# Optimization experiments

Measured on AMD Instinct MI355X. Metric: run time of the kernel, lower is better.

The kernel has to match this reference:

```python
import jax, jax.numpy as jnp
import numpy as np

TAU_U = 1.0
TAU_L = 0.05
EPS = 1e-12  # torch F.normalize eps


def setup_inputs() -> dict:
    key = jax.random.key(0)
    ks = jax.random.split(key, 8)
    N, D, B = 100000, 128, 8192
    x1 = jax.random.normal(ks[0], (N, D), dtype=jnp.float32)
    x2 = jax.random.normal(ks[1], (N, D), dtype=jnp.float32)
    x1_index = jax.random.randint(ks[2], (B,), 0, N, dtype=jnp.int64 if jax.config.jax_enable_x64 else jnp.int32)
    x2_index = jax.random.randint(ks[3], (B,), 0, N, dtype=jnp.int64 if jax.config.jax_enable_x64 else jnp.int32)
    # Linear params (torch Linear default init: U(-1/sqrt(fan_in), 1/sqrt(fan_in)))
    lim1 = 1.0 / np.sqrt(D)
    W1 = jax.random.uniform(ks[4], (D, D), minval=-lim1, maxval=lim1, dtype=jnp.float32)
    b1 = jax.random.uniform(ks[5], (D,), minval=-lim1, maxval=lim1, dtype=jnp.float32)
    W2 = jax.random.uniform(ks[6], (1, D), minval=-lim1, maxval=lim1, dtype=jnp.float32)
    b2 = jax.random.uniform(ks[7], (1,), minval=-lim1, maxval=lim1, dtype=jnp.float32)
    return {"x1": x1, "x2": x2, "x1_index": x1_index, "x2_index": x2_index,
            "W1": W1, "b1": b1, "W2": W2, "b2": b2}


def _l2norm(x):
    # matches torch F.normalize(dim=1) for 2-D input
    n = jnp.sqrt(jnp.sum(x * x, axis=-1, keepdims=True))
    return x / jnp.maximum(n, EPS)


def reference(x1, x2, x1_index, x2_index, W1, b1, W2, b2):
    x1_feat = _l2norm(x1[x1_index])          # [B, D]
    x2_feat = _l2norm(x2[x2_index])          # [B, D]

    h = x1_feat * x2_feat                    # [B, D]
    h = h @ W1.T + b1                        # lin1
    h = jnp.where(h >= 0, h, 0.2 * h)        # leaky_relu(0.2)
    s = jax.nn.sigmoid(h @ W2.T + b2)        # [B, 1]
    ssl_temp = (TAU_U - TAU_L) * (1.0 - s) + TAU_L   # [B, 1]

    pos = jnp.sum(x1_feat * x2_feat, axis=-1)         # [B]
    # NOTE: [B] / [B,1] broadcasts to [B,B] exactly like torch
    pos_rating = jnp.exp(pos / ssl_temp)              # [B, B]

    tot = x1_feat @ x2_feat.T                          # [B, B]
    tot_rating = jnp.sum(jnp.exp(tot / ssl_temp), axis=1)  # [B]

    ssl_temp_avg = jnp.mean(ssl_temp)
    return (pos_rating, tot_rating, ssl_temp_avg)
```

## Files before the change

kernel.cpp:

```cpp
#include <hip/hip_runtime.h>
#include <stdint.h>

typedef __bf16 bf16x8 __attribute__((ext_vector_type(8)));
typedef float f32x4 __attribute__((ext_vector_type(4)));
typedef __attribute__((address_space(3))) uint32_t as3u32;
typedef const __attribute__((address_space(1))) uint32_t as1u32;

#define B_TOT 8192
#define DD 128
#define OUT_TOT 67108864UL
#define OUT_AVG 67117056UL

__device__ inline unsigned short f2bf(float x){
  union { float f; uint32_t u; } v; v.f = x;
  return (unsigned short)((v.u + 0x7fffu + ((v.u >> 16) & 1u)) >> 16);
}

__global__ __launch_bounds__(256) void k_feat(const float* __restrict__ x1,
    const float* __restrict__ x2, const int* __restrict__ i1a, const int* __restrict__ i2a,
    unsigned short* __restrict__ f1b, unsigned short* __restrict__ f2b,
    unsigned short* __restrict__ hb, float* __restrict__ posw, float* __restrict__ out){
  int tid = threadIdx.x;
  int gid = blockIdx.x * 256 + tid;
  if (gid <= 8192) out[OUT_TOT + gid] = 0.f;
  int w = tid >> 6, l = tid & 63;
  int b = blockIdx.x * 4 + w;
  const float2* r1 = (const float2*)(x1 + (size_t)i1a[b] * DD);
  const float2* r2 = (const float2*)(x2 + (size_t)i2a[b] * DD);
  float2 v1 = r1[l], v2 = r2[l];
  float s1 = v1.x * v1.x + v1.y * v1.y;
  float s2 = v2.x * v2.x + v2.y * v2.y;
  #pragma unroll
  for (int o = 32; o; o >>= 1){ s1 += __shfl_xor(s1, o); s2 += __shfl_xor(s2, o); }
  float inv1 = 1.f / fmaxf(sqrtf(s1), 1e-12f);
  float inv2 = 1.f / fmaxf(sqrtf(s2), 1e-12f);
  float f1x = v1.x * inv1, f1y = v1.y * inv1;
  float f2x = v2.x * inv2, f2y = v2.y * inv2;
  float hx = f1x * f2x, hy = f1y * f2y;
  float ps = hx + hy;
  #pragma unroll
  for (int o = 32; o; o >>= 1) ps += __shfl_xor(ps, o);
  unsigned int u1 = (unsigned int)f2bf(f1x) | ((unsigned int)f2bf(f1y) << 16);
  unsigned int u2 = (unsigned int)f2bf(f2x) | ((unsigned int)f2bf(f2y) << 16);
  unsigned int uh = (unsigned int)f2bf(hx)  | ((unsigned int)f2bf(hy)  << 16);
  ((unsigned int*)f1b)[b * 64 + l] = u1;
  ((unsigned int*)f2b)[b * 64 + l] = u2;
  ((unsigned int*)hb)[b * 64 + l]  = uh;
  if (l == 0) posw[b] = ps;
}

__device__ inline void stage_tile(const unsigned short* g, unsigned short* s){
  int tid = threadIdx.x;
  #pragma unroll
  for (int it = 0; it < 8; ++it){
    int c = tid + it * 256;
    int row = c >> 4, cc = c & 15;
    int src = (row << 4) + (cc ^ (row & 7));
    __builtin_amdgcn_global_load_lds((as1u32*)(g + src * 8),
                                     (as3u32*)(s + c * 8), 16, 0, 0);
  }
}

__device__ inline void mfma_tile(const unsigned short* As, const unsigned short* Bs,
                                 f32x4 acc[4][4]){
  int tid = threadIdx.x;
  int w = tid >> 6, l = tid & 63;
  int wr = (w >> 1) * 64, wc = (w & 1) * 64;
  int lo = l & 15, hi = l >> 4;
  f32x4 zero = {0.f, 0.f, 0.f, 0.f};
  #pragma unroll
  for (int m = 0; m < 4; ++m)
    #pragma unroll
    for (int n = 0; n < 4; ++n) acc[m][n] = zero;
  #pragma unroll
  for (int kk = 0; kk < 4; ++kk){
    bf16x8 af[4], bfv[4];
    #pragma unroll
    for (int m = 0; m < 4; ++m){
      int row = wr + m * 16 + lo;
      af[m] = *(const bf16x8*)(As + row * 128 + ((kk * 4 + hi) ^ (row & 7)) * 8);
    }
    #pragma unroll
    for (int n = 0; n < 4; ++n){
      int row = wc + n * 16 + lo;
      bfv[n] = *(const bf16x8*)(Bs + row * 128 + ((kk * 4 + hi) ^ (row & 7)) * 8);
    }
    #pragma unroll
    for (int m = 0; m < 4; ++m)
      #pragma unroll
      for (int n = 0; n < 4; ++n)
        acc[m][n] = __builtin_amdgcn_mfma_f32_16x16x32_bf16(af[m], bfv[n], acc[m][n], 0, 0, 0);
  }
}

__global__ __launch_bounds__(256) void k_lin(const unsigned short* __restrict__ hb,
    const float* __restrict__ W1, const float* __restrict__ b1,
    const float* __restrict__ W2, const float* __restrict__ b2,
    float* __restrict__ rTw, float* __restrict__ out){
  __shared__ __align__(16) unsigned short As[16384];
  __shared__ __align__(16) unsigned short Bs[16384];
  __shared__ float zpart[2][128];
  __shared__ float s4[4];
  int i0 = blockIdx.x * 128;
  int tid = threadIdx.x;
  stage_tile(hb + (size_t)i0 * 128, As);
  #pragma unroll
  for (int it = 0; it < 8; ++it){
    int c = tid + it * 256;
    int row = c >> 4, cc = c & 15;
    int src = (row << 4) + (cc ^ (row & 7));
    const float4* g4 = (const float4*)(W1 + src * 8);
    float4 a = g4[0], b = g4[1];
    unsigned short t8[8];
    t8[0] = f2bf(a.x); t8[1] = f2bf(a.y); t8[2] = f2bf(a.z); t8[3] = f2bf(a.w);
    t8[4] = f2bf(b.x); t8[5] = f2bf(b.y); t8[6] = f2bf(b.z); t8[7] = f2bf(b.w);
    *(uint4*)(Bs + c * 8) = *(uint4*)t8;
  }
  asm volatile("s_waitcnt vmcnt(0)" ::: "memory");
  __syncthreads();
  f32x4 acc[4][4];
  mfma_tile(As, Bs, acc);
  int w = tid >> 6, l = tid & 63;
  int wrb = (w >> 1) * 64, wcb = (w & 1) * 64, lo = l & 15, hi = l >> 4;
  float w2v[4], b1v[4];
  #pragma unroll
  for (int n = 0; n < 4; ++n){ int col = wcb + n * 16 + lo; w2v[n] = W2[col]; b1v[n] = b1[col]; }
  #pragma unroll
  for (int m = 0; m < 4; ++m){
    #pragma unroll
    for (int q = 0; q < 4; ++q){
      float p = 0.f;
      #pragma unroll
      for (int n = 0; n < 4; ++n){
        float hv = acc[m][n][q] + b1v[n];
        hv = hv >= 0.f ? hv : 0.2f * hv;
        p += hv * w2v[n];
      }
      p += __shfl_xor(p, 1); p += __shfl_xor(p, 2);
      p += __shfl_xor(p, 4); p += __shfl_xor(p, 8);
      if (lo == 0) zpart[w & 1][wrb + m * 16 + hi * 4 + q] = p;
    }
  }
  __syncthreads();
  float Tloc = 0.f;
  if (tid < 128){
    float z = zpart[0][tid] + zpart[1][tid] + b2[0];
    float s = 1.f / (1.f + __expf(-z));
    float T = 0.95f * (1.f - s) + 0.05f;
    rTw[i0 + tid] = 1.f / T;
    Tloc = T;
  }
  float v = Tloc;
  #pragma unroll
  for (int o = 32; o; o >>= 1) v += __shfl_xor(v, o);
  if ((tid & 63) == 0) s4[tid >> 6] = v;
  __syncthreads();
  if (tid == 0) atomicAdd(out + OUT_AVG, (s4[0] + s4[1] + s4[2] + s4[3]) * (1.0f / 8192.0f));
}

__global__ __launch_bounds__(256, 2) void k_tot(const unsigned short* __restrict__ f1b,
    const unsigned short* __restrict__ f2b, const float* __restrict__ rTw,
    float* __restrict__ out){
  __shared__ __align__(16) unsigned short Buf[16384];
  __shared__ __align__(16) float rS[128];
  int s = (blockIdx.x & 7) * 64 + (blockIdx.x >> 3);
  int rt = s & 63, ctg = s >> 6;
  int tid = threadIdx.x, w = tid >> 6, l = tid & 63;
  int wr = (w >> 1) * 64, wc = (w & 1) * 64;
  int lo = l & 15, hi = l >> 4;
  stage_tile(f1b + (size_t)rt * 16384, Buf);
  if (tid < 32)
    __builtin_amdgcn_global_load_lds((as1u32*)(rTw + rt * 128 + tid * 4),
                                     (as3u32*)(rS + tid * 4), 16, 0, 0);
  asm volatile("s_waitcnt vmcnt(0)" ::: "memory");
  __builtin_amdgcn_s_barrier();
  bf16x8 af[4][4];
  #pragma unroll
  for (int kk = 0; kk < 4; ++kk)
    #pragma unroll
    for (int m = 0; m < 4; ++m){
      int row = wr + m * 16 + lo;
      af[kk][m] = *(const bf16x8*)(Buf + row * 128 + ((kk * 4 + hi) ^ (row & 7)) * 8);
    }
  asm volatile("s_waitcnt lgkmcnt(0)" ::: "memory");
  __builtin_amdgcn_s_barrier();
  stage_tile(f2b + (size_t)(ctg * 8) * 16384, Buf);
  asm volatile("s_waitcnt vmcnt(0)" ::: "memory");
  __builtin_amdgcn_s_barrier();
  float pacc[4][4] = {{0.f,0.f,0.f,0.f},{0.f,0.f,0.f,0.f},{0.f,0.f,0.f,0.f},{0.f,0.f,0.f,0.f}};
  #pragma unroll 1
  for (int c8 = 0; c8 < 8; ++c8){
    int ct = ctg * 8 + c8;
    f32x4 acc[4][4];
    f32x4 zero = {0.f,0.f,0.f,0.f};
    #pragma unroll
    for (int m = 0; m < 4; ++m)
      #pragma unroll
      for (int n = 0; n < 4; ++n) acc[m][n] = zero;
    #pragma unroll
    for (int kk = 0; kk < 4; ++kk){
      bf16x8 bfv[4];
      #pragma unroll
      for (int n = 0; n < 4; ++n){
        int row = wc + n * 16 + lo;
        bfv[n] = *(const bf16x8*)(Buf + row * 128 + ((kk * 4 + hi) ^ (row & 7)) * 8);
      }
      #pragma unroll
      for (int m = 0; m < 4; ++m)
        #pragma unroll
        for (int n = 0; n < 4; ++n)
          acc[m][n] = __builtin_amdgcn_mfma_f32_16x16x32_bf16(af[kk][m], bfv[n], acc[m][n], 0, 0, 0);
    }
    asm volatile("s_waitcnt lgkmcnt(0)" ::: "memory");
    __builtin_amdgcn_s_barrier();
    if (c8 < 7) stage_tile(f2b + (size_t)(ct + 1) * 16384, Buf);
    #pragma unroll
    for (int m = 0; m < 4; ++m)
      #pragma unroll
      for (int q = 0; q < 4; ++q){
        float r = rS[wr + m * 16 + hi * 4 + q];
        pacc[m][q] += __expf(acc[m][0][q] * r) + __expf(acc[m][1][q] * r)
                    + __expf(acc[m][2][q] * r) + __expf(acc[m][3][q] * r);
      }
    if (c8 < 7){
      asm volatile("s_waitcnt vmcnt(0)" ::: "memory");
      __builtin_amdgcn_s_barrier();
    }
  }
  #pragma unroll
  for (int m = 0; m < 4; ++m)
    #pragma unroll
    for (int q = 0; q < 4; ++q){
      float p = pacc[m][q];
      p += __shfl_xor(p, 1); p += __shfl_xor(p, 2);
      p += __shfl_xor(p, 4); p += __shfl_xor(p, 8);
      if (lo == 0) atomicAdd(out + OUT_TOT + rt * 128 + wr + m * 16 + hi * 4 + q, p);
    }
}

__global__ __launch_bounds__(256) void k_pr(const float* __restrict__ posw,
    const float* __restrict__ rTw, float* __restrict__ out){
  int tid = threadIdx.x;
  int r0 = blockIdx.x * 4;
  f32x4 p[8];
  #pragma unroll
  for (int c = 0; c < 8; ++c) p[c] = *(const f32x4*)(posw + (c * 256 + tid) * 4);
  float4 rr4 = *(const float4*)(rTw + r0);
  float rr[4] = {rr4.x, rr4.y, rr4.z, rr4.w};
  #pragma unroll
  for (int r = 0; r < 4; ++r){
    float* ob = out + (size_t)(r0 + r) * B_TOT;
    #pragma unroll
    for (int c = 0; c < 8; ++c){
      f32x4 e;
      e.x = __expf(p[c].x * rr[r]); e.y = __expf(p[c].y * rr[r]);
      e.z = __expf(p[c].z * rr[r]); e.w = __expf(p[c].w * rr[r]);
      *(f32x4*)(ob + (c * 256 + tid) * 4) = e;
    }
  }
}

extern "C" void kernel_launch(void* const* d_in, const int* in_sizes, int n_in,
                              void* d_out, int out_size, void* d_ws, size_t ws_size,
                              hipStream_t stream){
  const float* x1 = (const float*)d_in[0];
  const float* x2 = (const float*)d_in[1];
  const int*   i1 = (const int*)d_in[2];
  const int*   i2 = (const int*)d_in[3];
  const float* W1 = (const float*)d_in[4];
  const float* b1 = (const float*)d_in[5];
  const float* W2 = (const float*)d_in[6];
  const float* b2 = (const float*)d_in[7];
  float* out = (float*)d_out;
  char* ws = (char*)d_ws;
  unsigned short* hb   = (unsigned short*)(ws);
  unsigned short* f1b  = (unsigned short*)(ws + 2097152);
  unsigned short* f2b  = (unsigned short*)(ws + 4194304);
  float* posw  = (float*)(ws + 6291456);
  float* rTw   = (float*)(ws + 6324224);

  hipLaunchKernelGGL(k_feat,  dim3(2048), dim3(256), 0, stream, x1, x2, i1, i2, f1b, f2b, hb, posw, out);
  hipLaunchKernelGGL(k_lin,   dim3(64),   dim3(256), 0, stream, hb, W1, b1, W2, b2, rTw, out);
  hipLaunchKernelGGL(k_tot,   dim3(512),  dim3(256), 0, stream, f1b, f2b, rTw, out);
  hipLaunchKernelGGL(k_pr,    dim3(2048), dim3(256), 0, stream, posw, rTw, out);
}
```

Measured before the change: 86.56 us.

## Spread lin1 over more blocks with fp32 W1 and halve column tiles per tot block

The small lin1 kernel moves from 64 blocks doing a bf16 MFMA tile to 512 blocks, each handling 16 rows with scalar fp32 dot products against W1 staged in LDS. This removes the on-the-fly bf16 conversion of W1 and keeps W1 in full precision. The tot kernel doubles its grid to 1024 blocks, each covering 4 column tiles instead of 8, to raise occupancy and balance across CUs. In exchange, each f1 row tile is reloaded more often, atomics on the row sums double, and every lin1 block reloads the full 64KB W1.

```diff
diff --git a/kernel.cpp b/kernel.cpp
--- a/kernel.cpp
+++ b/kernel.cpp
@@ -14,6 +14,9 @@
 __device__ inline unsigned short f2bf(float x){
   union { float f; uint32_t u; } v; v.f = x;
   return (unsigned short)((v.u + 0x7fffu + ((v.u >> 16) & 1u)) >> 16);
+}
+__device__ inline float bf2f(unsigned short u){
+  union { uint32_t u; float f; } v; v.u = (uint32_t)u << 16; return v.f;
 }
 
 __global__ __launch_bounds__(256) void k_feat(const float* __restrict__ x1,
@@ -61,101 +64,62 @@
   }
 }
 
-__device__ inline void mfma_tile(const unsigned short* As, const unsigned short* Bs,
-                                 f32x4 acc[4][4]){
-  int tid = threadIdx.x;
-  int w = tid >> 6, l = tid & 63;
-  int wr = (w >> 1) * 64, wc = (w & 1) * 64;
-  int lo = l & 15, hi = l >> 4;
-  f32x4 zero = {0.f, 0.f, 0.f, 0.f};
-  #pragma unroll
-  for (int m = 0; m < 4; ++m)
-    #pragma unroll
-    for (int n = 0; n < 4; ++n) acc[m][n] = zero;
-  #pragma unroll
-  for (int kk = 0; kk < 4; ++kk){
-    bf16x8 af[4], bfv[4];
-    #pragma unroll
-    for (int m = 0; m < 4; ++m){
-      int row = wr + m * 16 + lo;
-      af[m] = *(const bf16x8*)(As + row * 128 + ((kk * 4 + hi) ^ (row & 7)) * 8);
-    }
-    #pragma unroll
-    for (int n = 0; n < 4; ++n){
-      int row = wc + n * 16 + lo;
-      bfv[n] = *(const bf16x8*)(Bs + row * 128 + ((kk * 4 + hi) ^ (row & 7)) * 8);
-    }
-    #pragma unroll
-    for (int m = 0; m < 4; ++m)
-      #pragma unroll
-      for (int n = 0; n < 4; ++n)
-        acc[m][n] = __builtin_amdgcn_mfma_f32_16x16x32_bf16(af[m], bfv[n], acc[m][n], 0, 0, 0);
-  }
-}
-
 __global__ __launch_bounds__(256) void k_lin(const unsigned short* __restrict__ hb,
     const float* __restrict__ W1, const float* __restrict__ b1,
     const float* __restrict__ W2, const float* __restrict__ b2,
     float* __restrict__ rTw, float* __restrict__ out){
-  __shared__ __align__(16) unsigned short As[16384];
-  __shared__ __align__(16) unsigned short Bs[16384];
-  __shared__ float zpart[2][128];
+  __shared__ __align__(16) float W1S[16384];
+  __shared__ __align__(16) unsigned short hS[2048];
   __shared__ float s4[4];
-  int i0 = blockIdx.x * 128;
-  int tid = threadIdx.x;
-  stage_tile(hb + (size_t)i0 * 128, As);
-  #pragma unroll
-  for (int it = 0; it < 8; ++it){
+  int tid = threadIdx.x;
+  int i0 = blockIdx.x * 16;
+  #pragma unroll
+  for (int it = 0; it < 16; ++it){
     int c = tid + it * 256;
-    int row = c >> 4, cc = c & 15;
-    int src = (row << 4) + (cc ^ (row & 7));
-    const float4* g4 = (const float4*)(W1 + src * 8);
-    float4 a = g4[0], b = g4[1];
-    unsigned short t8[8];
-    t8[0] = f2bf(a.x); t8[1] = f2bf(a.y); t8[2] = f2bf(a.z); t8[3] = f2bf(a.w);
-    t8[4] = f2bf(b.x); t8[5] = f2bf(b.y); t8[6] = f2bf(b.z); t8[7] = f2bf(b.w);
-    *(uint4*)(Bs + c * 8) = *(uint4*)t8;
-  }
+    __builtin_amdgcn_global_load_lds((as1u32*)(W1 + c * 4), (as3u32*)(W1S + c * 4), 16, 0, 0);
+  }
+  __builtin_amdgcn_global_load_lds((as1u32*)(hb + (size_t)i0 * 128 + tid * 8),
+                                   (as3u32*)(hS + tid * 8), 16, 0, 0);
   asm volatile("s_waitcnt vmcnt(0)" ::: "memory");
   __syncthreads();
-  f32x4 acc[4][4];
-  mfma_tile(As, Bs, acc);
-  int w = tid >> 6, l = tid & 63;
-  int wrb = (w >> 1) * 64, wcb = (w & 1) * 64, lo = l & 15, hi = l >> 4;
-  float w2v[4], b1v[4];
-  #pragma unroll
-  for (int n = 0; n < 4; ++n){ int col = wcb + n * 16 + lo; w2v[n] = W2[col]; b1v[n] = b1[col]; }
-  #pragma unroll
-  for (int m = 0; m < 4; ++m){
-    #pragma unroll
-    for (int q = 0; q < 4; ++q){
-      float p = 0.f;
-      #pragma unroll
-      for (int n = 0; n < 4; ++n){
-        float hv = acc[m][n][q] + b1v[n];
-        hv = hv >= 0.f ? hv : 0.2f * hv;
-        p += hv * w2v[n];
-      }
-      p += __shfl_xor(p, 1); p += __shfl_xor(p, 2);
-      p += __shfl_xor(p, 4); p += __shfl_xor(p, 8);
-      if (lo == 0) zpart[w & 1][wrb + m * 16 + hi * 4 + q] = p;
-    }
-  }
+  int l = tid & 63;
+  int r = tid >> 4;
+  int j0 = (tid & 15) * 8;
+  float acc[8] = {0.f,0.f,0.f,0.f,0.f,0.f,0.f,0.f};
+  int kq0 = ((l & 15) * 2 + (l >> 4)) & 31;
+  #pragma unroll 4
+  for (int i = 0; i < 32; ++i){
+    int kq = (kq0 + i) & 31;
+    ushort4 hu = *(const ushort4*)(hS + r * 128 + kq * 4);
+    float h0 = bf2f(hu.x), h1 = bf2f(hu.y), h2 = bf2f(hu.z), h3 = bf2f(hu.w);
+    #pragma unroll
+    for (int jj = 0; jj < 8; ++jj){
+      f32x4 wq = *(const f32x4*)(W1S + (j0 + jj) * 128 + kq * 4);
+      acc[jj] += h0 * wq.x + h1 * wq.y + h2 * wq.z + h3 * wq.w;
+    }
+  }
+  float p = 0.f;
+  #pragma unroll
+  for (int jj = 0; jj < 8; ++jj){
+    int j = j0 + jj;
+    float z = acc[jj] + b1[j];
+    z = z >= 0.f ? z : 0.2f * z;
+    p += z * W2[j];
+  }
+  p += __shfl_xor(p, 1); p += __shfl_xor(p, 2);
+  p += __shfl_xor(p, 4); p += __shfl_xor(p, 8);
+  float T = 0.f;
+  if ((tid & 15) == 0){
+    float z2 = p + b2[0];
+    float s = 1.f / (1.f + __expf(-z2));
+    T = 0.95f * (1.f - s) + 0.05f;
+    rTw[i0 + r] = 1.f / T;
+  }
+  float v = T;
+  v += __shfl_xor(v, 16); v += __shfl_xor(v, 32);
+  if (l == 0) s4[tid >> 6] = v;
   __syncthreads();
-  float Tloc = 0.f;
-  if (tid < 128){
-    float z = zpart[0][tid] + zpart[1][tid] + b2[0];
-    float s = 1.f / (1.f + __expf(-z));
-    float T = 0.95f * (1.f - s) + 0.05f;
-    rTw[i0 + tid] = 1.f / T;
-    Tloc = T;
-  }
-  float v = Tloc;
-  #pragma unroll
-  for (int o = 32; o; o >>= 1) v += __shfl_xor(v, o);
-  if ((tid & 63) == 0) s4[tid >> 6] = v;
-  __syncthreads();
-  if (tid == 0) atomicAdd(out + OUT_AVG, (s4[0] + s4[1] + s4[2] + s4[3]) * (1.0f / 8192.0f));
+  if (tid == 0) atomicAdd(out + OUT_AVG, (s4[0]+s4[1]+s4[2]+s4[3]) * (1.f/8192.f));
 }
 
 __global__ __launch_bounds__(256, 2) void k_tot(const unsigned short* __restrict__ f1b,
@@ -163,8 +127,9 @@
     float* __restrict__ out){
   __shared__ __align__(16) unsigned short Buf[16384];
   __shared__ __align__(16) float rS[128];
-  int s = (blockIdx.x & 7) * 64 + (blockIdx.x >> 3);
-  int rt = s & 63, ctg = s >> 6;
+  int g = blockIdx.x;
+  int s = (g & 7) * 128 + (g >> 3);
+  int rt = s & 63, cg = s >> 6;
   int tid = threadIdx.x, w = tid >> 6, l = tid & 63;
   int wr = (w >> 1) * 64, wc = (w & 1) * 64;
   int lo = l & 15, hi = l >> 4;
@@ -184,13 +149,13 @@
     }
   asm volatile("s_waitcnt lgkmcnt(0)" ::: "memory");
   __builtin_amdgcn_s_barrier();
-  stage_tile(f2b + (size_t)(ctg * 8) * 16384, Buf);
+  stage_tile(f2b + (size_t)(cg * 4) * 16384, Buf);
   asm volatile("s_waitcnt vmcnt(0)" ::: "memory");
   __builtin_amdgcn_s_barrier();
   float pacc[4][4] = {{0.f,0.f,0.f,0.f},{0.f,0.f,0.f,0.f},{0.f,0.f,0.f,0.f},{0.f,0.f,0.f,0.f}};
   #pragma unroll 1
-  for (int c8 = 0; c8 < 8; ++c8){
-    int ct = ctg * 8 + c8;
+  for (int c4 = 0; c4 < 4; ++c4){
+    int ct = cg * 4 + c4;
     f32x4 acc[4][4];
     f32x4 zero = {0.f,0.f,0.f,0.f};
     #pragma unroll
@@ -213,7 +178,7 @@
     }
     asm volatile("s_waitcnt lgkmcnt(0)" ::: "memory");
     __builtin_amdgcn_s_barrier();
-    if (c8 < 7) stage_tile(f2b + (size_t)(ct + 1) * 16384, Buf);
+    if (c4 < 3) stage_tile(f2b + (size_t)(ct + 1) * 16384, Buf);
     #pragma unroll
     for (int m = 0; m < 4; ++m)
       #pragma unroll
@@ -222,7 +187,7 @@
         pacc[m][q] += __expf(acc[m][0][q] * r) + __expf(acc[m][1][q] * r)
                     + __expf(acc[m][2][q] * r) + __expf(acc[m][3][q] * r);
       }
-    if (c8 < 7){
+    if (c4 < 3){
       asm volatile("s_waitcnt vmcnt(0)" ::: "memory");
       __builtin_amdgcn_s_barrier();
     }
@@ -279,8 +244,8 @@
   float* posw  = (float*)(ws + 6291456);
   float* rTw   = (float*)(ws + 6324224);
 
-  hipLaunchKernelGGL(k_feat,  dim3(2048), dim3(256), 0, stream, x1, x2, i1, i2, f1b, f2b, hb, posw, out);
-  hipLaunchKernelGGL(k_lin,   dim3(64),   dim3(256), 0, stream, hb, W1, b1, W2, b2, rTw, out);
-  hipLaunchKernelGGL(k_tot,   dim3(512),  dim3(256), 0, stream, f1b, f2b, rTw, out);
-  hipLaunchKernelGGL(k_pr,    dim3(2048), dim3(256), 0, stream, posw, rTw, out);
-}
+  hipLaunchKernelGGL(k_feat, dim3(2048), dim3(256), 0, stream, x1, x2, i1, i2, f1b, f2b, hb, posw, out);
+  hipLaunchKernelGGL(k_lin,  dim3(512),  dim3(256), 0, stream, hb, W1, b1, W2, b2, rTw, out);
+  hipLaunchKernelGGL(k_tot,  dim3(1024), dim3(256), 0, stream, f1b, f2b, rTw, out);
+  hipLaunchKernelGGL(k_pr,   dim3(2048), dim3(256), 0, stream, posw, rTw, out);
+}
```

New measurement: 94.96 us. 1.1x slower.

## Double-buffer B tiles in k_tot with separate A buffer and 64-row stages

Applied to the files above, without the earlier changes.

Gives A its own LDS buffer and splits the B stream into two 64-row buffers, so the load of the next B sub-tile overlaps MFMA and exp work on the current one. Before, one shared buffer forced a full vmcnt(0) wait and barrier after every 128-column tile. The loop now runs 16 iterations with a vmcnt(4) partial wait. In exchange each iteration does less MFMA work per barrier, and LDS use rises from 32KB to 64KB per block, which may limit how many blocks fit per CU at launch bounds of 2.

```diff
diff --git a/kernel.cpp b/kernel.cpp
--- a/kernel.cpp
+++ b/kernel.cpp
@@ -53,6 +53,17 @@
   int tid = threadIdx.x;
   #pragma unroll
   for (int it = 0; it < 8; ++it){
+    int c = tid + it * 256;
+    int row = c >> 4, cc = c & 15;
+    int src = (row << 4) + (cc ^ (row & 7));
+    __builtin_amdgcn_global_load_lds((as1u32*)(g + src * 8),
+                                     (as3u32*)(s + c * 8), 16, 0, 0);
+  }
+}
+__device__ inline void stage_tile64(const unsigned short* g, unsigned short* s){
+  int tid = threadIdx.x;
+  #pragma unroll
+  for (int it = 0; it < 4; ++it){
     int c = tid + it * 256;
     int row = c >> 4, cc = c & 15;
     int src = (row << 4) + (cc ^ (row & 7));
@@ -161,17 +172,22 @@
 __global__ __launch_bounds__(256, 2) void k_tot(const unsigned short* __restrict__ f1b,
     const unsigned short* __restrict__ f2b, const float* __restrict__ rTw,
     float* __restrict__ out){
-  __shared__ __align__(16) unsigned short Buf[16384];
+  __shared__ __align__(16) unsigned short Abuf[16384];
+  __shared__ __align__(16) unsigned short Bbuf0[8192];
+  __shared__ __align__(16) unsigned short Bbuf1[8192];
   __shared__ __align__(16) float rS[128];
   int s = (blockIdx.x & 7) * 64 + (blockIdx.x >> 3);
   int rt = s & 63, ctg = s >> 6;
   int tid = threadIdx.x, w = tid >> 6, l = tid & 63;
-  int wr = (w >> 1) * 64, wc = (w & 1) * 64;
+  int wr = (w >> 1) * 64, wc = (w & 1) * 32;
   int lo = l & 15, hi = l >> 4;
-  stage_tile(f1b + (size_t)rt * 16384, Buf);
+  const unsigned short* Bg = f2b + (size_t)(ctg * 1024) * 128;
+  stage_tile(f1b + (size_t)rt * 16384, Abuf);
   if (tid < 32)
     __builtin_amdgcn_global_load_lds((as1u32*)(rTw + rt * 128 + tid * 4),
                                      (as3u32*)(rS + tid * 4), 16, 0, 0);
+  stage_tile64(Bg, Bbuf0);
+  stage_tile64(Bg + 64 * 128, Bbuf1);
   asm volatile("s_waitcnt vmcnt(0)" ::: "memory");
   __builtin_amdgcn_s_barrier();
   bf16x8 af[4][4];
@@ -180,52 +196,45 @@
     #pragma unroll
     for (int m = 0; m < 4; ++m){
       int row = wr + m * 16 + lo;
-      af[kk][m] = *(const bf16x8*)(Buf + row * 128 + ((kk * 4 + hi) ^ (row & 7)) * 8);
-    }
-  asm volatile("s_waitcnt lgkmcnt(0)" ::: "memory");
-  __builtin_amdgcn_s_barrier();
-  stage_tile(f2b + (size_t)(ctg * 8) * 16384, Buf);
-  asm volatile("s_waitcnt vmcnt(0)" ::: "memory");
-  __builtin_amdgcn_s_barrier();
+      af[kk][m] = *(const bf16x8*)(Abuf + row * 128 + ((kk * 4 + hi) ^ (row & 7)) * 8);
+    }
   float pacc[4][4] = {{0.f,0.f,0.f,0.f},{0.f,0.f,0.f,0.f},{0.f,0.f,0.f,0.f},{0.f,0.f,0.f,0.f}};
+  unsigned short* ba = Bbuf0;
+  unsigned short* bb = Bbuf1;
   #pragma unroll 1
-  for (int c8 = 0; c8 < 8; ++c8){
-    int ct = ctg * 8 + c8;
-    f32x4 acc[4][4];
+  for (int i = 0; i < 16; ++i){
+    if (i < 15) asm volatile("s_waitcnt vmcnt(4)" ::: "memory");
+    else        asm volatile("s_waitcnt vmcnt(0)" ::: "memory");
+    __builtin_amdgcn_s_barrier();
+    f32x4 acc[4][2];
     f32x4 zero = {0.f,0.f,0.f,0.f};
     #pragma unroll
-    for (int m = 0; m < 4; ++m)
-      #pragma unroll
-      for (int n = 0; n < 4; ++n) acc[m][n] = zero;
+    for (int m = 0; m < 4; ++m){ acc[m][0] = zero; acc[m][1] = zero; }
     #pragma unroll
     for (int kk = 0; kk < 4; ++kk){
-      bf16x8 bfv[4];
-      #pragma unroll
-      for (int n = 0; n < 4; ++n){
+      bf16x8 bfv[2];
+      #pragma unroll
+      for (int n = 0; n < 2; ++n){
         int row = wc + n * 16 + lo;
-        bfv[n] = *(const bf16x8*)(Buf + row * 128 + ((kk * 4 + hi) ^ (row & 7)) * 8);
-      }
-      #pragma unroll
-      for (int m = 0; m < 4; ++m)
-        #pragma unroll
-        for (int n = 0; n < 4; ++n)
-          acc[m][n] = __builtin_amdgcn_mfma_f32_16x16x32_bf16(af[kk][m], bfv[n], acc[m][n], 0, 0, 0);
+        bfv[n] = *(const bf16x8*)(ba + row * 128 + ((kk * 4 + hi) ^ (row & 7)) * 8);
+      }
+      #pragma unroll
+      for (int m = 0; m < 4; ++m){
+        acc[m][0] = __builtin_amdgcn_mfma_f32_16x16x32_bf16(af[kk][m], bfv[0], acc[m][0], 0, 0, 0);
+        acc[m][1] = __builtin_amdgcn_mfma_f32_16x16x32_bf16(af[kk][m], bfv[1], acc[m][1], 0, 0, 0);
+      }
     }
     asm volatile("s_waitcnt lgkmcnt(0)" ::: "memory");
     __builtin_amdgcn_s_barrier();
-    if (c8 < 7) stage_tile(f2b + (size_t)(ct + 1) * 16384, Buf);
+    if (i < 14) stage_tile64(Bg + (size_t)(i + 2) * 64 * 128, ba);
     #pragma unroll
     for (int m = 0; m < 4; ++m)
       #pragma unroll
       for (int q = 0; q < 4; ++q){
         float r = rS[wr + m * 16 + hi * 4 + q];
-        pacc[m][q] += __expf(acc[m][0][q] * r) + __expf(acc[m][1][q] * r)
-                    + __expf(acc[m][2][q] * r) + __expf(acc[m][3][q] * r);
-      }
-    if (c8 < 7){
-      asm volatile("s_waitcnt vmcnt(0)" ::: "memory");
-      __builtin_amdgcn_s_barrier();
-    }
+        pacc[m][q] += __expf(acc[m][0][q] * r) + __expf(acc[m][1][q] * r);
+      }
+    unsigned short* t = ba; ba = bb; bb = t;
   }
   #pragma unroll
   for (int m = 0; m < 4; ++m)
@@ -279,8 +288,8 @@
   float* posw  = (float*)(ws + 6291456);
   float* rTw   = (float*)(ws + 6324224);
 
-  hipLaunchKernelGGL(k_feat,  dim3(2048), dim3(256), 0, stream, x1, x2, i1, i2, f1b, f2b, hb, posw, out);
-  hipLaunchKernelGGL(k_lin,   dim3(64),   dim3(256), 0, stream, hb, W1, b1, W2, b2, rTw, out);
-  hipLaunchKernelGGL(k_tot,   dim3(512),  dim3(256), 0, stream, f1b, f2b, rTw, out);
-  hipLaunchKernelGGL(k_pr,    dim3(2048), dim3(256), 0, stream, posw, rTw, out);
-}
+  hipLaunchKernelGGL(k_feat, dim3(2048), dim3(256), 0, stream, x1, x2, i1, i2, f1b, f2b, hb, posw, out);
+  hipLaunchKernelGGL(k_lin,  dim3(64),   dim3(256), 0, stream, hb, W1, b1, W2, b2, rTw, out);
+  hipLaunchKernelGGL(k_tot,  dim3(512),  dim3(256), 0, stream, f1b, f2b, rTw, out);
+  hipLaunchKernelGGL(k_pr,   dim3(2048), dim3(256), 0, stream, posw, rTw, out);
+}
```

After: 87.68 us. Within noise of the previous version (+1.3%).
